# Optimization experiments

Hardware: AMD Instinct MI355X
Metric: run time of the kernel (lower is better)

The kernel has to match this reference:

```python
import jax, jax.numpy as jnp
import numpy as np

H, W = 160, 160
FS = 7
SPAN = FS // 2
NUM_CLASSES = 19
NUM_ITERS = 5
THETA_ALPHA = 160.0  # scales rgb in bilateral features
THETA_BETA = 3.0     # scales position in bilateral features
THETA_GAMMA = 3.0    # scales position in spatial features
EPS = 1e-20

# offsets ordered (dx outer, dy inner) to match TF filter-tap index (dx+span)*FS + (dy+span)
OFFSETS = [(dx, dy) for dx in range(-SPAN, SPAN + 1) for dy in range(-SPAN, SPAN + 1)]


def _make_filter(features):
    # features: (bs, cf, H, W) -> gaussian affinity filter (bs, FS*FS, H, W)
    # filter[b, k, i, j] = exp(-0.5 * ||f[b,:,i+dx,j+dy] - f[b,:,i,j]||^2), 0 if out of bounds
    fp = jnp.pad(features, ((0, 0), (0, 0), (SPAN, SPAN), (SPAN, SPAN)))
    rows = jnp.arange(H)
    cols = jnp.arange(W)
    taps = []
    for dx, dy in OFFSETS:
        shifted = fp[:, :, SPAN + dx:SPAN + dx + H, SPAN + dy:SPAN + dy + W]
        aff = jnp.exp(-0.5 * jnp.sum((features - shifted) ** 2, axis=1))  # (bs, H, W)
        mask = (((rows + dx >= 0) & (rows + dx < H))[:, None]
                & ((cols + dy >= 0) & (cols + dy < W))[None, :])
        taps.append(aff * mask)
    return jnp.stack(taps, axis=1)  # (bs, FS*FS, H, W)


def _patches(x):
    # x: (bs, C, H, W) -> (bs, C, FS*FS, H, W), zero-padded shifts (matches extract_patches SAME)
    xp = jnp.pad(x, ((0, 0), (0, 0), (SPAN, SPAN), (SPAN, SPAN)))
    return jnp.stack(
        [xp[:, :, SPAN + dx:SPAN + dx + H, SPAN + dy:SPAN + dy + W] for dx, dy in OFFSETS],
        axis=2)


def _compute_gaussian(x, filt):
    # x: (bs, C, H, W), filt: (bs, FS*FS, H, W) -> (bs, C, H, W)
    return jnp.sum(_patches(x) * filt[:, None], axis=2)


def _forward(unaries, rgb, spatial_ker_weights, bilateral_ker_weights, compatibility_matrix):
    u = jnp.transpose(unaries, (0, 3, 1, 2))     # (bs, C, H, W)
    rgb_nchw = jnp.transpose(rgb, (0, 3, 1, 2))  # (bs, 3, H, W)
    bs = u.shape[0]
    mesh = jnp.stack(
        jnp.meshgrid(jnp.arange(H, dtype=jnp.float32), jnp.arange(W, dtype=jnp.float32),
                     indexing='ij'), 0)          # (2, H, W)
    spatial_feat = jnp.broadcast_to((mesh / THETA_GAMMA)[None], (bs, 2, H, W))
    bilateral_feat = jnp.concatenate(
        [rgb_nchw / THETA_ALPHA,
         jnp.broadcast_to((mesh / THETA_BETA)[None], (bs, 2, H, W))], axis=1)  # (bs, 5, H, W)

    spatial_filter = _make_filter(spatial_feat)
    bilateral_filter = _make_filter(bilateral_feat)

    ones = jnp.ones_like(u)
    spatial_norm = _compute_gaussian(ones, spatial_filter)
    bilateral_norm = _compute_gaussian(ones, bilateral_filter)

    q = u
    for _ in range(NUM_ITERS):
        # NOTE: original code does tf.nn.softmax(q_values, 0) -> softmax over the BATCH axis.
        sm = jax.nn.softmax(q, axis=0)
        s_out = _compute_gaussian(sm, spatial_filter) / (spatial_norm + EPS)
        b_out = _compute_gaussian(sm, bilateral_filter) / (bilateral_norm + EPS)
        msg = (jnp.einsum('kc,bchw->bkhw', spatial_ker_weights, s_out)
               + jnp.einsum('kc,bchw->bkhw', bilateral_ker_weights, b_out))
        pairwise = jnp.einsum('kc,bchw->bkhw', compatibility_matrix, msg)
        q = u - pairwise
    return jnp.transpose(q, (0, 2, 3, 1))  # (bs, H, W, C)


def setup_inputs() -> dict:
    key = jax.random.key(0)
    k1, k2 = jax.random.split(key)
    unaries = jax.random.normal(k1, (2, H, W, NUM_CLASSES), dtype=jnp.float32)
    rgb = jax.random.uniform(k2, (2, H, W, 3), dtype=jnp.float32) * 255.0
    eye = jnp.eye(NUM_CLASSES, dtype=jnp.float32)
    return {
        'unaries': unaries,
        'rgb': rgb,
        'spatial_ker_weights': eye,            # _diagonal_initializer
        'bilateral_ker_weights': eye,          # _diagonal_initializer
        'compatibility_matrix': -eye,          # _potts_model_initializer
    }


def reference(unaries, rgb, spatial_ker_weights, bilateral_ker_weights, compatibility_matrix):
    return _forward(unaries, rgb, spatial_ker_weights, bilateral_ker_weights,
                    compatibility_matrix)
```

## Files before the change

kernel.cpp:

```cpp
#include <hip/hip_runtime.h>


typedef __attribute__((ext_vector_type(4))) _Float16 half4;
typedef __attribute__((ext_vector_type(2))) _Float16 half2f;
typedef __attribute__((ext_vector_type(4))) float float4v;

#define HH 160
#define WW 160
#define NPIX (HH*WW)
#define NC 19
#define NG 5
#define SPAN 3
#define TR 8
#define TC 16
#define NPXT 128
#define LR 14
#define LC 22
#define LCP 24
#define HSTRIDE (LR*LCP)
#define NHALO (LR*LC)
#define NRING 180
#define NBLK 200
#define NTHR 640
#define EPSF 1e-20f
#define MAGICV 0x5EEDF00Du

#define BAR_CNT(k) (32 + (k)*32)
#define BAR_REL    288

#define SZ_A    30720
#define OFF_WB  SZ_A
#define SHM_SZ  (SZ_A + 25*128*8)

__device__ __forceinline__ float fast_rcp(float x) { return __builtin_amdgcn_rcpf(x); }

__device__ __forceinline__ float smx0(float q0, float q1) {
    const float m  = fmaxf(q0, q1);
    const float e0 = __expf(q0 - m);
    const float e1 = __expf(q1 - m);
    return e0 * fast_rcp(e0 + e1);
}

__global__ void __launch_bounds__(NTHR) crf_kernel(
        const float* __restrict__ u,
        const float* __restrict__ rgb,
        const float* __restrict__ sw,
        const float* __restrict__ bw,
        const float* __restrict__ compat,
        unsigned long long* __restrict__ gsmA,
        unsigned long long* __restrict__ gsmB,
        unsigned* __restrict__ bar,
        float* __restrict__ out) {
    __shared__ __align__(16) char shm[SHM_SZ];
    __shared__ float Msh[960];
    __shared__ float rowsum[NC];
    __shared__ int   diagflag;
    float4*   rgbL = (float4*)shm;
    half4*    smH  = (half4*)shm;
    float*    accF = (float*)shm;
    unsigned* wbW  = (unsigned*)(shm + OFF_WB);
    const uint2* wbP = (const uint2*)(shm + OFF_WB);

    constexpr float WSPC[49] = {
        0.36787944f,0.48567179f,0.57375342f,0.60653066f,0.57375342f,0.48567179f,0.36787944f,
        0.48567179f,0.64118039f,0.75746513f,0.80073740f,0.75746513f,0.64118039f,0.48567179f,
        0.57375342f,0.75746513f,0.89483932f,0.94595947f,0.89483932f,0.75746513f,0.57375342f,
        0.60653066f,0.80073740f,0.94595947f,1.00000000f,0.94595947f,0.80073740f,0.60653066f,
        0.57375342f,0.75746513f,0.89483932f,0.94595947f,0.89483932f,0.75746513f,0.57375342f,
        0.48567179f,0.64118039f,0.75746513f,0.80073740f,0.75746513f,0.64118039f,0.48567179f,
        0.36787944f,0.48567179f,0.57375342f,0.60653066f,0.57375342f,0.48567179f,0.36787944f };

    const int tid = threadIdx.x;
    const int px  = tid & 127;
    const int g   = tid >> 7;
    const int r   = px >> 4, c = px & 15;
    const int ti0 = blockIdx.y * TR, tj0 = blockIdx.x * TC;
    const int gp  = (ti0 + r) * WW + (tj0 + c);
    const int ctr = (r + SPAN) * LCP + (c + SPAN);
    const int ku  = 4 * g;
    const int bid = blockIdx.y * 10 + blockIdx.x;

    if (bid == 0 && tid == 0) {
        #pragma unroll
        for (int k = 0; k < 8; ++k)
            __hip_atomic_store(&bar[BAR_CNT(k)], 0u, __ATOMIC_RELAXED, __HIP_MEMORY_SCOPE_AGENT);
        __hip_atomic_store(&bar[BAR_REL], 0u, __ATOMIC_RELAXED, __HIP_MEMORY_SCOPE_AGENT);
        __hip_atomic_store(&bar[0], MAGICV, __ATOMIC_RELEASE, __HIP_MEMORY_SCOPE_AGENT);
    }
    if (tid == 0) {
        diagflag = 1;
        while (__hip_atomic_load(&bar[0], __ATOMIC_ACQUIRE, __HIP_MEMORY_SCOPE_AGENT) != MAGICV)
            __builtin_amdgcn_s_sleep(2);
    }
    if (tid < NC) {
        float rs = 0.0f;
        for (int cb = 0; cb < NC; ++cb) rs += sw[tid*NC + cb] + bw[tid*NC + cb];
        rowsum[tid] = rs;
    }
    __syncthreads();

    for (int e = tid; e < 960; e += NTHR) {
        const int k = e / 48, cc2 = e % 48;
        float acc = 0.0f;
        if (k < NC) {
            if (cc2 < NC) {
                for (int j = 0; j < NC; ++j) acc += compat[k*NC + j] * sw[j*NC + cc2];
            } else if (cc2 >= 20 && cc2 < 20 + NC) {
                const int cb = cc2 - 20;
                for (int j = 0; j < NC; ++j) acc += compat[k*NC + j] * bw[j*NC + cb];
            } else if (cc2 == 40) {
                for (int j = 0; j < NC; ++j) acc += compat[k*NC + j] * rowsum[j];
            }
        }
        Msh[e] = acc;
        bool off = false;
        if (k < NC) {
            if (cc2 < NC && cc2 != k && acc != 0.0f) off = true;
            if (cc2 >= 20 && cc2 < 20 + NC && (cc2 - 20) != k && acc != 0.0f) off = true;
        }
        if (off) atomicAnd(&diagflag, 0);
    }
    __syncthreads();

    float dsv[4], dbv[4];
    #pragma unroll
    for (int i = 0; i < 4; ++i) {
        dsv[i] = Msh[(ku + i) * 48 + (ku + i)];
        dbv[i] = Msh[(ku + i) * 48 + 20 + (ku + i)];
    }
    const bool isdiag = (diagflag != 0);

    for (int e = tid; e < 2 * NHALO; e += NTHR) {
        const int bb = e / NHALO, pos = e % NHALO;
        const int hr = pos / LC, hc = pos % LC;
        const int yi = ti0 - SPAN + hr, xj = tj0 - SPAN + hc;
        float4 rv = make_float4(0.f, 0.f, 0.f, 0.f);
        if ((unsigned)yi < HH && (unsigned)xj < WW) {
            const float* p = rgb + ((size_t)(bb * NPIX) + yi * WW + xj) * 3;
            rv = make_float4(p[0]*(1.f/160.f), p[1]*(1.f/160.f), p[2]*(1.f/160.f), 1.f);
        }
        rgbL[(bb ? HSTRIDE : 0) + hr * LCP + hc] = rv;
    }
    __syncthreads();

    {
        const float4 cv0 = rgbL[ctr];
        const float4 cv1 = rgbL[HSTRIDE + ctr];
        const int tapb = g * 10;
        const int ntap = (g == 4) ? 9 : 10;
        for (int i = 0; i < ntap; ++i) {
            const int t = tapb + i;
            const int dx = t / 7 - SPAN, dy = t % 7 - SPAN;
            const int n = ctr + dx * LCP + dy;
            const float4 nv0 = rgbL[n];
            const float4 nv1 = rgbL[HSTRIDE + n];
            const float wsm = __expf(-(float)(dx*dx + dy*dy) * (1.f/18.f)) * nv0.w;
            const float dr0 = cv0.x-nv0.x, dg0 = cv0.y-nv0.y, db0 = cv0.z-nv0.z;
            const float dr1 = cv1.x-nv1.x, dg1 = cv1.y-nv1.y, db1 = cv1.z-nv1.z;
            const float wb0 = wsm * __expf(-0.5f*(dr0*dr0+dg0*dg0+db0*db0));
            const float wb1 = wsm * __expf(-0.5f*(dr1*dr1+dg1*dg1+db1*db1));
            half2f hw = {(_Float16)wb0, (_Float16)wb1};
            unsigned uw; __builtin_memcpy(&uw, &hw, 4);
            wbW[(t >> 1) * 256 + px * 2 + (t & 1)] = uw;
        }
        if (g == 4) wbW[24 * 256 + px * 2 + 1] = 0u;
    }
    __syncthreads();

    float snI, bnI0, bnI1;
    {
        float sn = 0.f, bn0 = 0.f, bn1 = 0.f;
        #pragma unroll
        for (int t = 0; t < 49; ++t) {
            const unsigned uw = wbW[(t >> 1) * 256 + px * 2 + (t & 1)];
            half2f hw; __builtin_memcpy(&hw, &uw, 4);
            bn0 += (float)hw.x; bn1 += (float)hw.y;
            const int dx = t / 7 - SPAN, dy = t % 7 - SPAN;
            const int yi = ti0 + r + dx, xj = tj0 + c + dy;
            sn += (((unsigned)yi < HH) && ((unsigned)xj < WW)) ? WSPC[t] : 0.0f;
        }
        snI  = fast_rcp(sn + EPSF);
        bnI0 = fast_rcp(bn0 + EPSF);
        bnI1 = fast_rcp(bn1 + EPSF);
    }

    float uv0[4], uv1[4];
    #pragma unroll
    for (int i = 0; i < 4; ++i) {
        const int ch = 4*g + i;
        uv0[i] = (ch < NC) ? u[(size_t)gp * NC + ch] : 0.0f;
        uv1[i] = (ch < NC) ? u[((size_t)NPIX + gp) * NC + ch] : 0.0f;
    }

    for (int it = 0; it < 5; ++it) {
        if (it > 0) {
            __syncthreads();
            if (tid == 0) {
                __hip_atomic_fetch_add(&bar[BAR_CNT(bid & 7)], 1u,
                                       __ATOMIC_RELAXED, __HIP_MEMORY_SCOPE_AGENT);
                if (bid == 0) {
                    unsigned sum;
                    do {
                        sum = 0;
                        #pragma unroll
                        for (int k = 0; k < 8; ++k)
                            sum += __hip_atomic_load(&bar[BAR_CNT(k)],
                                                     __ATOMIC_RELAXED, __HIP_MEMORY_SCOPE_AGENT);
                        if (sum < (unsigned)(NBLK * it)) __builtin_amdgcn_s_sleep(2);
                    } while (sum < (unsigned)(NBLK * it));
                    __hip_atomic_store(&bar[BAR_REL], (unsigned)it,
                                       __ATOMIC_RELAXED, __HIP_MEMORY_SCOPE_AGENT);
                } else {
                    while (__hip_atomic_load(&bar[BAR_REL],
                                             __ATOMIC_RELAXED, __HIP_MEMORY_SCOPE_AGENT)
                           < (unsigned)it)
                        __builtin_amdgcn_s_sleep(2);
                }
            }
            __syncthreads();
        }

        const unsigned long long* gsrc = ((it & 1) ? gsmA : gsmB);
        if (it == 0) {
            #pragma unroll
            for (int k2 = 0; k2 < 3; ++k2) {
                const int e = tid + NTHR * k2;
                if (e < NG * NHALO) {
                    const int sg = e / NHALO, pos = e - sg * NHALO;
                    const int hr = pos / LC, hc = pos - hr * LC;
                    const int yi = ti0 - SPAN + hr, xj = tj0 - SPAN + hc;
                    half4 hv = (half4)(_Float16)0.0f;
                    if ((unsigned)yi < HH && (unsigned)xj < WW) {
                        const int p = yi * WW + xj;
                        const float* q0 = u + (size_t)p * NC;
                        const float* q1 = u + (size_t)(NPIX + p) * NC;
                        #pragma unroll
                        for (int i = 0; i < 4; ++i) {
                            const int ch = 4*sg + i;
                            const float a = (ch < NC) ? q0[ch] : 0.0f;
                            const float d = (ch < NC) ? q1[ch] : 0.0f;
                            hv[i] = (_Float16)smx0(a, d);
                        }
                    }
                    smH[sg * HSTRIDE + hr * LCP + hc] = hv;
                }
            }
        } else if (isdiag) {
            #pragma unroll
            for (int k2 = 0; k2 < 2; ++k2) {
                const int e = tid + NTHR * k2;
                if (e < NG * NRING) {
                    const int sg = e / NRING, re = e - sg * NRING;
                    int hr, hc;
                    if (re < 66)        { hr = re / 22;          hc = re % 22; }
                    else if (re < 132)  { const int t2 = re - 66;  hr = 11 + t2 / 22; hc = t2 % 22; }
                    else                { const int t2 = re - 132; hr = 3 + t2 / 6;
                                          const int s = t2 % 6;    hc = (s < 3) ? s : s + 16; }
                    const int yi = ti0 - SPAN + hr, xj = tj0 - SPAN + hc;
                    half4 hv = (half4)(_Float16)0.0f;
                    if ((unsigned)yi < HH && (unsigned)xj < WW) {
                        const unsigned long long raw =
                            __hip_atomic_load(&gsrc[sg * NPIX + yi * WW + xj],
                                              __ATOMIC_RELAXED, __HIP_MEMORY_SCOPE_AGENT);
                        __builtin_memcpy(&hv, &raw, 8);
                    }
                    smH[sg * HSTRIDE + hr * LCP + hc] = hv;
                }
            }
        } else {
            #pragma unroll
            for (int k2 = 0; k2 < 3; ++k2) {
                const int e = tid + NTHR * k2;
                if (e < NG * NHALO) {
                    const int sg = e / NHALO, pos = e - sg * NHALO;
                    const int hr = pos / LC, hc = pos - hr * LC;
                    const int yi = ti0 - SPAN + hr, xj = tj0 - SPAN + hc;
                    half4 hv = (half4)(_Float16)0.0f;
                    if ((unsigned)yi < HH && (unsigned)xj < WW) {
                        const unsigned long long raw =
                            __hip_atomic_load(&gsrc[sg * NPIX + yi * WW + xj],
                                              __ATOMIC_RELAXED, __HIP_MEMORY_SCOPE_AGENT);
                        __builtin_memcpy(&hv, &raw, 8);
                    }
                    smH[sg * HSTRIDE + hr * LCP + hc] = hv;
                }
            }
        }
        __syncthreads();

        float4v sAv = (float4v)0.0f, b0a = (float4v)0.0f, b1a = (float4v)0.0f;
        const half4* pl = smH + g * HSTRIDE;
        #pragma unroll
        for (int i = 0; i < 24; ++i) {
            const uint2 wp = wbP[i * 128 + px];
            #pragma unroll
            for (int s = 0; s < 2; ++s) {
                const int t = 2*i + s;
                const int dx = t / 7 - SPAN, dy = t % 7 - SPAN;
                half2f hw; __builtin_memcpy(&hw, s ? &wp.y : &wp.x, 4);
                const float w0 = (float)hw.x, w1 = (float)hw.y;
                const half4 v = pl[ctr + dx*LCP + dy];
                const float4v f = {(float)v[0], (float)v[1], (float)v[2], (float)v[3]};
                sAv += WSPC[t] * f;
                b0a += w0 * f;
                b1a += w1 * f;
            }
        }
        {
            const uint2 wp = wbP[24 * 128 + px];
            half2f hw; __builtin_memcpy(&hw, &wp.x, 4);
            const float w0 = (float)hw.x, w1 = (float)hw.y;
            const half4 v = pl[ctr + SPAN*LCP + SPAN];
            const float4v f = {(float)v[0], (float)v[1], (float)v[2], (float)v[3]};
            sAv += WSPC[48] * f;
            b0a += w0 * f;
            b1a += w1 * f;
        }

        if (isdiag) {
            float q0v[4], q1v[4];
            #pragma unroll
            for (int i = 0; i < 4; ++i) {
                const float sAn = sAv[i] * snI;
                const float b0n = b0a[i] * bnI0;
                const float b1x = b1a[i] * bnI1;
                q0v[i] = uv0[i] - dsv[i]*sAn - dbv[i]*b0n;
                q1v[i] = uv1[i] - (dsv[i] + dbv[i]) + dsv[i]*sAn + dbv[i]*b1x;
            }
            if (it == 4) {
                #pragma unroll
                for (int i = 0; i < 4; ++i) {
                    const int ch = 4*g + i;
                    if (ch < NC) {
                        out[(size_t)gp * NC + ch]          = q0v[i];
                        out[((size_t)NPIX + gp) * NC + ch] = q1v[i];
                    }
                }
            } else {
                half4 sh;
                #pragma unroll
                for (int i = 0; i < 4; ++i) sh[i] = (_Float16)smx0(q0v[i], q1v[i]);
                __syncthreads();
                smH[g * HSTRIDE + ctr] = sh;
                unsigned long long u64; __builtin_memcpy(&u64, &sh, 8);
                unsigned long long* gdst = ((it & 1) ? gsmB : gsmA);
                __hip_atomic_store(&gdst[g * NPIX + gp], u64,
                                   __ATOMIC_RELAXED, __HIP_MEMORY_SCOPE_AGENT);
            }
        } else {
            float q0v[4], q1v[4];
            __syncthreads();
            #pragma unroll
            for (int i = 0; i < 4; ++i) {
                accF[(4*g + i) * NPXT + px]      = sAv[i] * snI;
                accF[(20 + 4*g + i) * NPXT + px] = b0a[i] * bnI0;
                accF[(40 + 4*g + i) * NPXT + px] = b1a[i] * bnI1;
            }
            __syncthreads();
            float t1[4] = {0,0,0,0}, t2[4] = {0,0,0,0}, t3[4] = {0,0,0,0};
            #pragma unroll
            for (int cc = 0; cc < 20; ++cc) {
                const float sv  = accF[cc * NPXT + px];
                const float b0v = accF[(20 + cc) * NPXT + px];
                const float b1v = accF[(40 + cc) * NPXT + px];
                #pragma unroll
                for (int i = 0; i < 4; ++i) {
                    const float* mk = Msh + (ku + i) * 48;
                    t1[i] += mk[cc] * sv;
                    t2[i] += mk[20 + cc] * b0v;
                    t3[i] += mk[20 + cc] * b1v;
                }
            }
            #pragma unroll
            for (int i = 0; i < 4; ++i) {
                const float rs = Msh[(ku + i) * 48 + 40];
                q0v[i] = uv0[i] - t1[i] - t2[i];
                q1v[i] = uv1[i] - rs + t1[i] + t3[i];
            }
            if (it == 4) {
                #pragma unroll
                for (int i = 0; i < 4; ++i) {
                    const int ch = 4*g + i;
                    if (ch < NC) {
                        out[(size_t)gp * NC + ch]          = q0v[i];
                        out[((size_t)NPIX + gp) * NC + ch] = q1v[i];
                    }
                }
            } else {
                half4 sh;
                #pragma unroll
                for (int i = 0; i < 4; ++i) sh[i] = (_Float16)smx0(q0v[i], q1v[i]);
                unsigned long long u64; __builtin_memcpy(&u64, &sh, 8);
                unsigned long long* gdst = ((it & 1) ? gsmB : gsmA);
                __hip_atomic_store(&gdst[g * NPIX + gp], u64,
                                   __ATOMIC_RELAXED, __HIP_MEMORY_SCOPE_AGENT);
            }
        }
    }
}

extern "C" void kernel_launch(void* const* d_in, const int* in_sizes, int n_in,
                              void* d_out, int out_size, void* d_ws, size_t ws_size,
                              hipStream_t stream) {
    const float* u      = (const float*)d_in[0];
    const float* rgb    = (const float*)d_in[1];
    const float* sw     = (const float*)d_in[2];
    const float* bw     = (const float*)d_in[3];
    const float* compat = (const float*)d_in[4];
    float* out = (float*)d_out;

    unsigned long long* gsmA = (unsigned long long*)d_ws;
    unsigned long long* gsmB = (unsigned long long*)((char*)d_ws + 1024000);
    unsigned* bar = (unsigned*)((char*)d_ws + 2048000);

    crf_kernel<<<dim3(WW/TC, HH/TR, 1), dim3(NTHR), 0, stream>>>(
        u, rgb, sw, bw, compat, gsmA, gsmB, bar, out);
}
```

Baseline: 110.8 us.

## Replace master-release grid barrier with all-poll barrier and unified halo exchange

```diff
diff --git a/kernel.cpp b/kernel.cpp
--- a/kernel.cpp
+++ b/kernel.cpp
@@ -26,7 +26,6 @@
 #define MAGICV 0x5EEDF00Du
 
 #define BAR_CNT(k) (32 + (k)*32)
-#define BAR_REL    288
 
 #define SZ_A    30720
 #define OFF_WB  SZ_A
@@ -84,7 +83,6 @@
         #pragma unroll
         for (int k = 0; k < 8; ++k)
             __hip_atomic_store(&bar[BAR_CNT(k)], 0u, __ATOMIC_RELAXED, __HIP_MEMORY_SCOPE_AGENT);
-        __hip_atomic_store(&bar[BAR_REL], 0u, __ATOMIC_RELAXED, __HIP_MEMORY_SCOPE_AGENT);
         __hip_atomic_store(&bar[0], MAGICV, __ATOMIC_RELEASE, __HIP_MEMORY_SCOPE_AGENT);
     }
     if (tid == 0) {
@@ -191,99 +189,55 @@
         uv0[i] = (ch < NC) ? u[(size_t)gp * NC + ch] : 0.0f;
         uv1[i] = (ch < NC) ? u[((size_t)NPIX + gp) * NC + ch] : 0.0f;
     }
+    half4 sh;
+    #pragma unroll
+    for (int i = 0; i < 4; ++i) sh[i] = (_Float16)smx0(uv0[i], uv1[i]);
 
     for (int it = 0; it < 5; ++it) {
-        if (it > 0) {
-            __syncthreads();
-            if (tid == 0) {
-                __hip_atomic_fetch_add(&bar[BAR_CNT(bid & 7)], 1u,
-                                       __ATOMIC_RELAXED, __HIP_MEMORY_SCOPE_AGENT);
-                if (bid == 0) {
-                    unsigned sum;
-                    do {
-                        sum = 0;
-                        #pragma unroll
-                        for (int k = 0; k < 8; ++k)
-                            sum += __hip_atomic_load(&bar[BAR_CNT(k)],
-                                                     __ATOMIC_RELAXED, __HIP_MEMORY_SCOPE_AGENT);
-                        if (sum < (unsigned)(NBLK * it)) __builtin_amdgcn_s_sleep(2);
-                    } while (sum < (unsigned)(NBLK * it));
-                    __hip_atomic_store(&bar[BAR_REL], (unsigned)it,
-                                       __ATOMIC_RELAXED, __HIP_MEMORY_SCOPE_AGENT);
-                } else {
-                    while (__hip_atomic_load(&bar[BAR_REL],
-                                             __ATOMIC_RELAXED, __HIP_MEMORY_SCOPE_AGENT)
-                           < (unsigned)it)
-                        __builtin_amdgcn_s_sleep(2);
+        {
+            unsigned long long u64; __builtin_memcpy(&u64, &sh, 8);
+            unsigned long long* gdst = ((it & 1) ? gsmB : gsmA);
+            __hip_atomic_store(&gdst[g * NPIX + gp], u64,
+                               __ATOMIC_RELAXED, __HIP_MEMORY_SCOPE_AGENT);
+        }
+        __syncthreads();
+        if (tid == 0) {
+            __hip_atomic_fetch_add(&bar[BAR_CNT(bid & 7)], 1u,
+                                   __ATOMIC_RELAXED, __HIP_MEMORY_SCOPE_AGENT);
+            const unsigned tgt = (unsigned)(NBLK * (it + 1));
+            unsigned sum;
+            do {
+                sum = 0;
+                #pragma unroll
+                for (int k = 0; k < 8; ++k)
+                    sum += __hip_atomic_load(&bar[BAR_CNT(k)],
+                                             __ATOMIC_RELAXED, __HIP_MEMORY_SCOPE_AGENT);
+                if (sum < tgt) __builtin_amdgcn_s_sleep(2);
+            } while (sum < tgt);
+        }
+        __syncthreads();
+
+        const unsigned long long* gsrc = ((it & 1) ? gsmB : gsmA);
+        smH[g * HSTRIDE + ctr] = sh;
+        #pragma unroll
+        for (int k2 = 0; k2 < 2; ++k2) {
+            const int e = tid + NTHR * k2;
+            if (e < NG * NRING) {
+                const int sg = e / NRING, re = e - sg * NRING;
+                int hr, hc;
+                if (re < 66)        { hr = re / 22;          hc = re % 22; }
+                else if (re < 132)  { const int t2 = re - 66;  hr = 11 + t2 / 22; hc = t2 % 22; }
+                else                { const int t2 = re - 132; hr = 3 + t2 / 6;
+                                      const int s = t2 % 6;    hc = (s < 3) ? s : s + 16; }
+                const int yi = ti0 - SPAN + hr, xj = tj0 - SPAN + hc;
+                half4 hv = (half4)(_Float16)0.0f;
+                if ((unsigned)yi < HH && (unsigned)xj < WW) {
+                    const unsigned long long raw =
+                        __hip_atomic_load(&gsrc[sg * NPIX + yi * WW + xj],
+                                          __ATOMIC_RELAXED, __HIP_MEMORY_SCOPE_AGENT);
+                    __builtin_memcpy(&hv, &raw, 8);
                 }
-            }
-            __syncthreads();
-        }
-
-        const unsigned long long* gsrc = ((it & 1) ? gsmA : gsmB);
-        if (it == 0) {
-            #pragma unroll
-            for (int k2 = 0; k2 < 3; ++k2) {
-                const int e = tid + NTHR * k2;
-                if (e < NG * NHALO) {
-                    const int sg = e / NHALO, pos = e - sg * NHALO;
-                    const int hr = pos / LC, hc = pos - hr * LC;
-                    const int yi = ti0 - SPAN + hr, xj = tj0 - SPAN + hc;
-                    half4 hv = (half4)(_Float16)0.0f;
-                    if ((unsigned)yi < HH && (unsigned)xj < WW) {
-                        const int p = yi * WW + xj;
-                        const float* q0 = u + (size_t)p * NC;
-                        const float* q1 = u + (size_t)(NPIX + p) * NC;
-                        #pragma unroll
-                        for (int i = 0; i < 4; ++i) {
-                            const int ch = 4*sg + i;
-                            const float a = (ch < NC) ? q0[ch] : 0.0f;
-                            const float d = (ch < NC) ? q1[ch] : 0.0f;
-                            hv[i] = (_Float16)smx0(a, d);
-                        }
-                    }
-                    smH[sg * HSTRIDE + hr * LCP + hc] = hv;
-                }
-            }
-        } else if (isdiag) {
-            #pragma unroll
-            for (int k2 = 0; k2 < 2; ++k2) {
-                const int e = tid + NTHR * k2;
-                if (e < NG * NRING) {
-                    const int sg = e / NRING, re = e - sg * NRING;
-                    int hr, hc;
-                    if (re < 66)        { hr = re / 22;          hc = re % 22; }
-                    else if (re < 132)  { const int t2 = re - 66;  hr = 11 + t2 / 22; hc = t2 % 22; }
-                    else                { const int t2 = re - 132; hr = 3 + t2 / 6;
-                                          const int s = t2 % 6;    hc = (s < 3) ? s : s + 16; }
-                    const int yi = ti0 - SPAN + hr, xj = tj0 - SPAN + hc;
-                    half4 hv = (half4)(_Float16)0.0f;
-                    if ((unsigned)yi < HH && (unsigned)xj < WW) {
-                        const unsigned long long raw =
-                            __hip_atomic_load(&gsrc[sg * NPIX + yi * WW + xj],
-                                              __ATOMIC_RELAXED, __HIP_MEMORY_SCOPE_AGENT);
-                        __builtin_memcpy(&hv, &raw, 8);
-                    }
-                    smH[sg * HSTRIDE + hr * LCP + hc] = hv;
-                }
-            }
-        } else {
-            #pragma unroll
-            for (int k2 = 0; k2 < 3; ++k2) {
-                const int e = tid + NTHR * k2;
-                if (e < NG * NHALO) {
-                    const int sg = e / NHALO, pos = e - sg * NHALO;
-                    const int hr = pos / LC, hc = pos - hr * LC;
-                    const int yi = ti0 - SPAN + hr, xj = tj0 - SPAN + hc;
-                    half4 hv = (half4)(_Float16)0.0f;
-                    if ((unsigned)yi < HH && (unsigned)xj < WW) {
-                        const unsigned long long raw =
-                            __hip_atomic_load(&gsrc[sg * NPIX + yi * WW + xj],
-                                              __ATOMIC_RELAXED, __HIP_MEMORY_SCOPE_AGENT);
-                        __builtin_memcpy(&hv, &raw, 8);
-                    }
-                    smH[sg * HSTRIDE + hr * LCP + hc] = hv;
-                }
+                smH[sg * HSTRIDE + hr * LCP + hc] = hv;
             }
         }
         __syncthreads();
@@ -317,8 +271,8 @@
             b1a += w1 * f;
         }
 
+        float q0v[4], q1v[4];
         if (isdiag) {
-            float q0v[4], q1v[4];
             #pragma unroll
             for (int i = 0; i < 4; ++i) {
                 const float sAn = sAv[i] * snI;
@@ -327,28 +281,7 @@
                 q0v[i] = uv0[i] - dsv[i]*sAn - dbv[i]*b0n;
                 q1v[i] = uv1[i] - (dsv[i] + dbv[i]) + dsv[i]*sAn + dbv[i]*b1x;
             }
-            if (it == 4) {
-                #pragma unroll
-                for (int i = 0; i < 4; ++i) {
-                    const int ch = 4*g + i;
-                    if (ch < NC) {
-                        out[(size_t)gp * NC + ch]          = q0v[i];
-                        out[((size_t)NPIX + gp) * NC + ch] = q1v[i];
-                    }
-                }
-            } else {
-                half4 sh;
-                #pragma unroll
-                for (int i = 0; i < 4; ++i) sh[i] = (_Float16)smx0(q0v[i], q1v[i]);
-                __syncthreads();
-                smH[g * HSTRIDE + ctr] = sh;
-                unsigned long long u64; __builtin_memcpy(&u64, &sh, 8);
-                unsigned long long* gdst = ((it & 1) ? gsmB : gsmA);
-                __hip_atomic_store(&gdst[g * NPIX + gp], u64,
-                                   __ATOMIC_RELAXED, __HIP_MEMORY_SCOPE_AGENT);
-            }
         } else {
-            float q0v[4], q1v[4];
             __syncthreads();
             #pragma unroll
             for (int i = 0; i < 4; ++i) {
@@ -377,24 +310,20 @@
                 q0v[i] = uv0[i] - t1[i] - t2[i];
                 q1v[i] = uv1[i] - rs + t1[i] + t3[i];
             }
-            if (it == 4) {
-                #pragma unroll
-                for (int i = 0; i < 4; ++i) {
-                    const int ch = 4*g + i;
-                    if (ch < NC) {
-                        out[(size_t)gp * NC + ch]          = q0v[i];
-                        out[((size_t)NPIX + gp) * NC + ch] = q1v[i];
-                    }
+        }
+
+        if (it == 4) {
+            #pragma unroll
+            for (int i = 0; i < 4; ++i) {
+                const int ch = 4*g + i;
+                if (ch < NC) {
+                    out[(size_t)gp * NC + ch]          = q0v[i];
+                    out[((size_t)NPIX + gp) * NC + ch] = q1v[i];
                 }
-            } else {
-                half4 sh;
-                #pragma unroll
-                for (int i = 0; i < 4; ++i) sh[i] = (_Float16)smx0(q0v[i], q1v[i]);
-                unsigned long long u64; __builtin_memcpy(&u64, &sh, 8);
-                unsigned long long* gdst = ((it & 1) ? gsmB : gsmA);
-                __hip_atomic_store(&gdst[g * NPIX + gp], u64,
-                                   __ATOMIC_RELAXED, __HIP_MEMORY_SCOPE_AGENT);
-            }
+            }
+        } else {
+            #pragma unroll
+            for (int i = 0; i < 4; ++i) sh[i] = (_Float16)smx0(q0v[i], q1v[i]);
         }
     }
 }
```

Result: no change. 111.5 us (+0.6%).
